# Kernel optimization log

Hardware: AMD Instinct MI355X
Metric: run time of the kernel (lower is better)

The kernel has to match this reference:

```python
import jax, jax.numpy as jnp
import numpy as np

B, T, D, H, HH, O = 1024, 1000, 6, 32, 15, 1


def _linear_params(key, fan_in, fan_out):
    k1, k2 = jax.random.split(key)
    s = 1.0 / np.sqrt(fan_in)
    W = jax.random.uniform(k1, (fan_in, fan_out), minval=-s, maxval=s, dtype=jnp.float32)
    b = jax.random.uniform(k2, (fan_out,), minval=-s, maxval=s, dtype=jnp.float32)
    return W, b


def setup_inputs() -> dict:
    key = jax.random.key(0)
    ks = jax.random.split(key, 7)
    W0, b0 = _linear_params(ks[0], D, H)        # initial_linear
    W1, b1 = _linear_params(ks[1], H, HH)       # vector field layer 1
    W2, b2 = _linear_params(ks[2], HH, HH)      # vector field layer 2
    W3, b3 = _linear_params(ks[3], HH, HH)      # vector field layer 3
    W4, b4 = _linear_params(ks[4], HH, H * D)   # output layer (tanh)
    Wf, bf = _linear_params(ks[5], H, O)        # final_linear
    coeffs = jax.random.normal(ks[6], (B, T, D), dtype=jnp.float32)
    return dict(coeffs=coeffs, W0=W0, b0=b0, W1=W1, b1=b1, W2=W2, b2=b2,
                W3=W3, b3=b3, W4=W4, b4=b4, Wf=Wf, bf=bf)


def reference(coeffs, W0, b0, W1, b1, W2, b2, W3, b3, W4, b4, Wf, bf):
    # h0 from initial values (use_initial=True, static_dim=None)
    h0 = coeffs[:, 0, :] @ W0 + b0  # [B, H]
    # linear interpolation on unit grid: dX/dt is piecewise constant per interval
    dX = jnp.transpose(coeffs[:, 1:, :] - coeffs[:, :-1, :], (1, 0, 2))  # [T-1, B, D]

    def vector_field(h):  # f(h): [B,H] -> [B,H,D]
        z = jax.nn.relu(h @ W1 + b1)
        z = jax.nn.relu(z @ W2 + b2)
        z = jax.nn.relu(z @ W3 + b3)
        return jnp.tanh(z @ W4 + b4).reshape(-1, H, D)

    def g(h, dx):  # f(h) dX/dt
        return jnp.einsum('bhd,bd->bh', vector_field(h), dx)

    def rk4_step(h, dx):  # classical RK4 over one unit interval
        k1 = g(h, dx)
        k2 = g(h + 0.5 * k1, dx)
        k3 = g(h + 0.5 * k2, dx)
        k4 = g(h + k3, dx)
        h_next = h + (k1 + 2.0 * k2 + 2.0 * k3 + k4) / 6.0
        return h_next, None

    hT, _ = jax.lax.scan(rk4_step, h0, dX)
    # return_sequences=False -> final linear on last hidden state
    return hT @ Wf + bf  # [B, O]
```

## Files before the change

### kernel.cpp

```cpp
#include <hip/hip_runtime.h>

#define BB  1024
#define TT  1000
#define DD  6
#define HN  32
#define HHN 15

__device__ __forceinline__ void pinf(float& v) { asm volatile("" : "+v"(v)); }

__device__ __forceinline__ float bcastf(float v, int l) {
    return __uint_as_float(__builtin_amdgcn_readlane(__float_as_uint(v), l));
}
__device__ __forceinline__ float qadd1(float v) {
    int t = __builtin_amdgcn_update_dpp(0, __float_as_int(v), 0xB1, 0xF, 0xF, true);
    return v + __int_as_float(t);
}
__device__ __forceinline__ float tanh_fast(float x) {
    float e = __builtin_amdgcn_exp2f(x * 2.885390081777927f);
    return fmaf(-2.0f, __builtin_amdgcn_rcpf(e + 1.0f), 1.0f);
}

extern "C" __global__ void __launch_bounds__(64)
__attribute__((amdgpu_waves_per_eu(1, 1)))
cde_kernel(const float* __restrict__ coeffs,
           const float* __restrict__ W0, const float* __restrict__ b0,
           const float* __restrict__ W1, const float* __restrict__ b1,
           const float* __restrict__ W2, const float* __restrict__ b2,
           const float* __restrict__ W3, const float* __restrict__ b3,
           const float* __restrict__ W4, const float* __restrict__ b4,
           const float* __restrict__ Wf, const float* __restrict__ bf,
           float* __restrict__ out)
{
    const int b = blockIdx.x;
    const int L = threadIdx.x;
    const float* cb = coeffs + (size_t)b * (TT * DD);

    const int quad = L >> 2;
    const int iq   = (quad < HHN) ? quad : (HHN - 1);
    const int par  = L & 1;

    float w1l[HN];
    #pragma unroll
    for (int k = 0; k < HN; ++k) { w1l[k] = W1[k * HHN + iq]; pinf(w1l[k]); }
    float w2l[HHN], w3l[HHN];
    #pragma unroll
    for (int k = 0; k < HHN; ++k) {
        w2l[k] = W2[k * HHN + iq]; pinf(w2l[k]);
        w3l[k] = W3[k * HHN + iq]; pinf(w3l[k]);
    }
    float bias1 = b1[iq]; pinf(bias1);
    float bias2 = b2[iq]; pinf(bias2);
    float bias3 = b3[iq]; pinf(bias3);

    float w4l[3][HHN], bias4[3];
    #pragma unroll
    for (int q = 0; q < 3; ++q) {
        const int c = 3 * L + q;
        bias4[q] = b4[c]; pinf(bias4[q]);
        #pragma unroll
        for (int k = 0; k < HHN; ++k) { w4l[q][k] = W4[k * (HN * DD) + c]; pinf(w4l[q][k]); }
    }

    const int j = L >> 1;
    float hd = b0[j];
    #pragma unroll
    for (int d = 0; d < DD; ++d) hd = fmaf(cb[d], W0[d * HN + j], hd);

    float xAl[3], xBl[3];
    #pragma unroll
    for (int e = 0; e < 3; ++e) { xAl[e] = cb[par * 3 + e]; xBl[e] = cb[DD + par * 3 + e]; }

    float ys[HN];
    float dxl[3];

    auto bcast32 = [&](float v) {
        #pragma unroll
        for (int k = 0; k < HN; ++k) ys[k] = bcastf(v, 2 * k);
    };

    auto evalg = [&]() -> float {
        float a0 = bias1, a1 = 0.f, a2 = 0.f, a3 = 0.f;
        #pragma unroll
        for (int k = 0; k < 8; ++k) {
            a0 = fmaf(ys[k],      w1l[k],      a0);
            a1 = fmaf(ys[k + 8],  w1l[k + 8],  a1);
            a2 = fmaf(ys[k + 16], w1l[k + 16], a2);
            a3 = fmaf(ys[k + 24], w1l[k + 24], a3);
        }
        const float z1 = fmaxf((a0 + a1) + (a2 + a3), 0.f);
        float zs[HHN];
        #pragma unroll
        for (int i = 0; i < HHN; ++i) zs[i] = bcastf(z1, 4 * i);

        float p0 = bias2, p1 = 0.f;
        #pragma unroll
        for (int k = 0; k < HHN - 1; k += 2) {
            p0 = fmaf(zs[k],     w2l[k],     p0);
            p1 = fmaf(zs[k + 1], w2l[k + 1], p1);
        }
        p0 = fmaf(zs[HHN - 1], w2l[HHN - 1], p0);
        const float z2 = fmaxf(p0 + p1, 0.f);
        #pragma unroll
        for (int i = 0; i < HHN; ++i) zs[i] = bcastf(z2, 4 * i);

        float q0 = bias3, q1 = 0.f;
        #pragma unroll
        for (int k = 0; k < HHN - 1; k += 2) {
            q0 = fmaf(zs[k],     w3l[k],     q0);
            q1 = fmaf(zs[k + 1], w3l[k + 1], q1);
        }
        q0 = fmaf(zs[HHN - 1], w3l[HHN - 1], q0);
        const float z3 = fmaxf(q0 + q1, 0.f);
        #pragma unroll
        for (int i = 0; i < HHN; ++i) zs[i] = bcastf(z3, 4 * i);

        float s0[3], s1[3];
        #pragma unroll
        for (int q = 0; q < 3; ++q) {
            s0[q] = bias4[q]; s1[q] = 0.f;
            #pragma unroll
            for (int k = 0; k < HHN - 1; k += 2) {
                s0[q] = fmaf(zs[k],     w4l[q][k],     s0[q]);
                s1[q] = fmaf(zs[k + 1], w4l[q][k + 1], s1[q]);
            }
            s0[q] = fmaf(zs[HHN - 1], w4l[q][HHN - 1], s0[q]);
        }
        float partial = 0.f;
        #pragma unroll
        for (int q = 0; q < 3; ++q)
            partial = fmaf(tanh_fast(s0[q] + s1[q]), dxl[q], partial);
        return qadd1(partial);
    };

    #pragma unroll 1
    for (int t = 0; t < TT - 1; ++t) {
        #pragma unroll
        for (int e = 0; e < 3; ++e) dxl[e] = xBl[e] - xAl[e];

        const int tn = (t + 2 < TT) ? (t + 2) : (TT - 1);
        float xNl[3];
        #pragma unroll
        for (int e = 0; e < 3; ++e) xNl[e] = cb[tn * DD + par * 3 + e];

        bcast32(hd);
        const float g1 = evalg();
        float acc = g1;
        float yd  = fmaf(0.5f, g1, hd);
        bcast32(yd);
        const float g2 = evalg();
        acc = fmaf(2.f, g2, acc);
        yd  = fmaf(0.5f, g2, hd);
        bcast32(yd);
        const float g3 = evalg();
        acc = fmaf(2.f, g3, acc);
        yd  = hd + g3;
        bcast32(yd);
        const float g4 = evalg();
        hd = fmaf(1.f / 6.f, acc + g4, hd);

        #pragma unroll
        for (int e = 0; e < 3; ++e) { xAl[e] = xBl[e]; xBl[e] = xNl[e]; }
    }

    float pz = hd * Wf[j] * 0.5f;
    #pragma unroll
    for (int off = 32; off > 0; off >>= 1) pz += __shfl_xor(pz, off);
    if (L == 0) out[b] = pz + bf[0];
}

extern "C" void kernel_launch(void* const* d_in, const int* in_sizes, int n_in,
                              void* d_out, int out_size, void* d_ws, size_t ws_size,
                              hipStream_t stream) {
    const float* coeffs = (const float*)d_in[0];
    const float* W0 = (const float*)d_in[1];
    const float* b0 = (const float*)d_in[2];
    const float* W1 = (const float*)d_in[3];
    const float* b1 = (const float*)d_in[4];
    const float* W2 = (const float*)d_in[5];
    const float* b2 = (const float*)d_in[6];
    const float* W3 = (const float*)d_in[7];
    const float* b3 = (const float*)d_in[8];
    const float* W4 = (const float*)d_in[9];
    const float* b4 = (const float*)d_in[10];
    const float* Wf = (const float*)d_in[11];
    const float* bf = (const float*)d_in[12];
    float* out = (float*)d_out;

    hipLaunchKernelGGL(cde_kernel, dim3(BB), dim3(64), 0, stream,
                       coeffs, W0, b0, W1, b1, W2, b2, W3, b3, W4, b4, Wf, bf, out);
}
```

Before: 1.480 ms.

## Pack MLP weights and activations to fp16 pairs and use dot2 with halved broadcasts

Stores the vector-field weights as packed fp16 pairs and uses v_dot2 fp16 dot products with fp32 accumulation, which halves the FMA count per layer. Activations are paired with a neighbouring lane through DPP and converted to packed fp16 before the readlane broadcast, so only half as many readlanes are needed per layer. Padding lanes get a -1e30 bias so they produce zeros after the ReLU. This lowers the latency of the serial RK4 chain but adds fp16 rounding to the hidden state and activations over 999 steps, which risks accuracy drift.

After: 1.193 ms. 1.24x faster.

```diff
diff --git a/kernel.cpp b/kernel.cpp
--- a/kernel.cpp
+++ b/kernel.cpp
@@ -6,10 +6,48 @@
 #define HN  32
 #define HHN 15
 
+typedef _Float16 h2 __attribute__((ext_vector_type(2)));
+typedef __fp16  fp16x2 __attribute__((ext_vector_type(2)));
+
 __device__ __forceinline__ void pinf(float& v) { asm volatile("" : "+v"(v)); }
-
-__device__ __forceinline__ float bcastf(float v, int l) {
-    return __uint_as_float(__builtin_amdgcn_readlane(__float_as_uint(v), l));
+__device__ __forceinline__ void pinh(h2& v) {
+    int t = __builtin_bit_cast(int, v);
+    asm volatile("" : "+v"(t));
+    v = __builtin_bit_cast(h2, t);
+}
+
+__device__ __forceinline__ h2 pkh_rtn(float a, float b) {
+    h2 r;
+    r.x = (_Float16)a;
+    r.y = (_Float16)b;
+    return r;
+}
+__device__ __forceinline__ h2 pkh(float a, float b) {
+    fp16x2 r = __builtin_amdgcn_cvt_pkrtz(a, b);
+    return __builtin_bit_cast(h2, r);
+}
+
+#if defined(__has_builtin)
+#if __has_builtin(__builtin_amdgcn_fdot2)
+#define HAVE_FDOT2 1
+#endif
+#endif
+__device__ __forceinline__ float dot2(h2 a, h2 b, float c) {
+#ifdef HAVE_FDOT2
+    return __builtin_amdgcn_fdot2(a, b, c, false);
+#else
+    return fmaf((float)a.x, (float)b.x, fmaf((float)a.y, (float)b.y, c));
+#endif
+}
+
+__device__ __forceinline__ h2 bch(h2 v, int l) {
+    return __builtin_bit_cast(h2, __builtin_amdgcn_readlane(__builtin_bit_cast(int, v), l));
+}
+__device__ __forceinline__ float dpp_xor2(float v) {
+    return __int_as_float(__builtin_amdgcn_update_dpp(0, __float_as_int(v), 0x4E, 0xF, 0xF, true));
+}
+__device__ __forceinline__ float dpp_shl4(float v) {
+    return __int_as_float(__builtin_amdgcn_update_dpp(0, __float_as_int(v), 0x104, 0xF, 0xF, true));
 }
 __device__ __forceinline__ float qadd1(float v) {
     int t = __builtin_amdgcn_update_dpp(0, __float_as_int(v), 0xB1, 0xF, 0xF, true);
@@ -39,26 +77,37 @@
     const int iq   = (quad < HHN) ? quad : (HHN - 1);
     const int par  = L & 1;
 
-    float w1l[HN];
-    #pragma unroll
-    for (int k = 0; k < HN; ++k) { w1l[k] = W1[k * HHN + iq]; pinf(w1l[k]); }
-    float w2l[HHN], w3l[HHN];
-    #pragma unroll
-    for (int k = 0; k < HHN; ++k) {
-        w2l[k] = W2[k * HHN + iq]; pinf(w2l[k]);
-        w3l[k] = W3[k * HHN + iq]; pinf(w3l[k]);
-    }
-    float bias1 = b1[iq]; pinf(bias1);
-    float bias2 = b2[iq]; pinf(bias2);
-    float bias3 = b3[iq]; pinf(bias3);
-
-    float w4l[3][HHN], bias4[3];
+    h2 w1p[16];
+    #pragma unroll
+    for (int m = 0; m < 16; ++m) {
+        w1p[m] = pkh_rtn(W1[(2 * m) * HHN + iq], W1[(2 * m + 1) * HHN + iq]);
+        pinh(w1p[m]);
+    }
+    h2 w2p[8], w3p[8];
+    #pragma unroll
+    for (int m = 0; m < 8; ++m) {
+        float a2 = W2[(2 * m) * HHN + iq];
+        float c2 = (2 * m + 1 < HHN) ? W2[(2 * m + 1) * HHN + iq] : 0.f;
+        w2p[m] = pkh_rtn(a2, c2); pinh(w2p[m]);
+        float a3 = W3[(2 * m) * HHN + iq];
+        float c3 = (2 * m + 1 < HHN) ? W3[(2 * m + 1) * HHN + iq] : 0.f;
+        w3p[m] = pkh_rtn(a3, c3); pinh(w3p[m]);
+    }
+    float bias1 = (quad < HHN) ? b1[iq] : -1e30f; pinf(bias1);
+    float bias2 = (quad < HHN) ? b2[iq] : -1e30f; pinf(bias2);
+    float bias3 = (quad < HHN) ? b3[iq] : -1e30f; pinf(bias3);
+
+    h2 w4p[3][8]; float bias4[3];
     #pragma unroll
     for (int q = 0; q < 3; ++q) {
         const int c = 3 * L + q;
         bias4[q] = b4[c]; pinf(bias4[q]);
         #pragma unroll
-        for (int k = 0; k < HHN; ++k) { w4l[q][k] = W4[k * (HN * DD) + c]; pinf(w4l[q][k]); }
+        for (int m = 0; m < 8; ++m) {
+            float a4 = W4[(2 * m) * (HN * DD) + c];
+            float c4 = (2 * m + 1 < HHN) ? W4[(2 * m + 1) * (HN * DD) + c] : 0.f;
+            w4p[q][m] = pkh_rtn(a4, c4); pinh(w4p[q][m]);
+        }
     }
 
     const int j = L >> 1;
@@ -70,65 +119,73 @@
     #pragma unroll
     for (int e = 0; e < 3; ++e) { xAl[e] = cb[par * 3 + e]; xBl[e] = cb[DD + par * 3 + e]; }
 
-    float ys[HN];
+    h2 sy[16];
     float dxl[3];
 
-    auto bcast32 = [&](float v) {
-        #pragma unroll
-        for (int k = 0; k < HN; ++k) ys[k] = bcastf(v, 2 * k);
+    auto uniy = [&](float yd) {
+        const float yp = dpp_xor2(yd);
+        const h2 ypk = pkh(yd, yp);
+        #pragma unroll
+        for (int m = 0; m < 16; ++m) sy[m] = bch(ypk, 4 * m);
     };
 
     auto evalg = [&]() -> float {
         float a0 = bias1, a1 = 0.f, a2 = 0.f, a3 = 0.f;
         #pragma unroll
-        for (int k = 0; k < 8; ++k) {
-            a0 = fmaf(ys[k],      w1l[k],      a0);
-            a1 = fmaf(ys[k + 8],  w1l[k + 8],  a1);
-            a2 = fmaf(ys[k + 16], w1l[k + 16], a2);
-            a3 = fmaf(ys[k + 24], w1l[k + 24], a3);
+        for (int m = 0; m < 4; ++m) {
+            a0 = dot2(sy[m],      w1p[m],      a0);
+            a1 = dot2(sy[m + 4],  w1p[m + 4],  a1);
+            a2 = dot2(sy[m + 8],  w1p[m + 8],  a2);
+            a3 = dot2(sy[m + 12], w1p[m + 12], a3);
         }
         const float z1 = fmaxf((a0 + a1) + (a2 + a3), 0.f);
-        float zs[HHN];
-        #pragma unroll
-        for (int i = 0; i < HHN; ++i) zs[i] = bcastf(z1, 4 * i);
+        h2 sz[8];
+        {
+            const float zp = dpp_shl4(z1);
+            const h2 zpk = pkh(z1, zp);
+            #pragma unroll
+            for (int m = 0; m < 8; ++m) sz[m] = bch(zpk, 8 * m);
+        }
 
         float p0 = bias2, p1 = 0.f;
         #pragma unroll
-        for (int k = 0; k < HHN - 1; k += 2) {
-            p0 = fmaf(zs[k],     w2l[k],     p0);
-            p1 = fmaf(zs[k + 1], w2l[k + 1], p1);
-        }
-        p0 = fmaf(zs[HHN - 1], w2l[HHN - 1], p0);
+        for (int m = 0; m < 4; ++m) {
+            p0 = dot2(sz[m],     w2p[m],     p0);
+            p1 = dot2(sz[m + 4], w2p[m + 4], p1);
+        }
         const float z2 = fmaxf(p0 + p1, 0.f);
-        #pragma unroll
-        for (int i = 0; i < HHN; ++i) zs[i] = bcastf(z2, 4 * i);
+        {
+            const float zp = dpp_shl4(z2);
+            const h2 zpk = pkh(z2, zp);
+            #pragma unroll
+            for (int m = 0; m < 8; ++m) sz[m] = bch(zpk, 8 * m);
+        }
 
         float q0 = bias3, q1 = 0.f;
         #pragma unroll
-        for (int k = 0; k < HHN - 1; k += 2) {
-            q0 = fmaf(zs[k],     w3l[k],     q0);
-            q1 = fmaf(zs[k + 1], w3l[k + 1], q1);
-        }
-        q0 = fmaf(zs[HHN - 1], w3l[HHN - 1], q0);
+        for (int m = 0; m < 4; ++m) {
+            q0 = dot2(sz[m],     w3p[m],     q0);
+            q1 = dot2(sz[m + 4], w3p[m + 4], q1);
+        }
         const float z3 = fmaxf(q0 + q1, 0.f);
-        #pragma unroll
-        for (int i = 0; i < HHN; ++i) zs[i] = bcastf(z3, 4 * i);
-
-        float s0[3], s1[3];
+        {
+            const float zp = dpp_shl4(z3);
+            const h2 zpk = pkh(z3, zp);
+            #pragma unroll
+            for (int m = 0; m < 8; ++m) sz[m] = bch(zpk, 8 * m);
+        }
+
+        float s[3];
         #pragma unroll
         for (int q = 0; q < 3; ++q) {
-            s0[q] = bias4[q]; s1[q] = 0.f;
-            #pragma unroll
-            for (int k = 0; k < HHN - 1; k += 2) {
-                s0[q] = fmaf(zs[k],     w4l[q][k],     s0[q]);
-                s1[q] = fmaf(zs[k + 1], w4l[q][k + 1], s1[q]);
-            }
-            s0[q] = fmaf(zs[HHN - 1], w4l[q][HHN - 1], s0[q]);
+            s[q] = bias4[q];
+            #pragma unroll
+            for (int m = 0; m < 8; ++m) s[q] = dot2(sz[m], w4p[q][m], s[q]);
         }
         float partial = 0.f;
         #pragma unroll
         for (int q = 0; q < 3; ++q)
-            partial = fmaf(tanh_fast(s0[q] + s1[q]), dxl[q], partial);
+            partial = fmaf(tanh_fast(s[q]), dxl[q], partial);
         return qadd1(partial);
     };
 
@@ -142,19 +199,19 @@
         #pragma unroll
         for (int e = 0; e < 3; ++e) xNl[e] = cb[tn * DD + par * 3 + e];
 
-        bcast32(hd);
+        uniy(hd);
         const float g1 = evalg();
         float acc = g1;
         float yd  = fmaf(0.5f, g1, hd);
-        bcast32(yd);
+        uniy(yd);
         const float g2 = evalg();
         acc = fmaf(2.f, g2, acc);
         yd  = fmaf(0.5f, g2, hd);
-        bcast32(yd);
+        uniy(yd);
         const float g3 = evalg();
         acc = fmaf(2.f, g3, acc);
         yd  = hd + g3;
-        bcast32(yd);
+        uniy(yd);
         const float g4 = evalg();
         hd = fmaf(1.f / 6.f, acc + g4, hd);
 
```
